# Optimization experiments

Hardware: AMD Instinct MI355X
Metric: run time of the kernel (lower is better)

## Reference

```python
import jax, jax.numpy as jnp
import numpy as np

D = 1024      # d_model
H = 2         # num_heads
DH = D // H   # head dim


def setup_inputs() -> dict:
    key = jax.random.key(0)
    ks = jax.random.split(key, 16)
    B, N = 512, 512
    s = 0.02
    return {
        "h": jax.random.normal(ks[0], (B, D), jnp.float32),
        "c": jax.random.normal(ks[1], (B, D), jnp.float32),
        "all_states": jax.random.normal(ks[2], (B, N, D), jnp.float32),
        "external_input": jax.random.normal(ks[3], (B, D), jnp.float32),
        # nn.MultiheadAttention params
        "in_proj_w": jax.random.normal(ks[4], (3 * D, D), jnp.float32) * s,
        "in_proj_b": jnp.zeros((3 * D,), jnp.float32),
        "out_proj_w": jax.random.normal(ks[5], (D, D), jnp.float32) * s,
        "out_proj_b": jnp.zeros((D,), jnp.float32),
        # nn.LSTMCell params (gate order: i, f, g, o)
        "w_ih": jax.random.normal(ks[6], (4 * D, 2 * D), jnp.float32) * s,
        "b_ih": jnp.zeros((4 * D,), jnp.float32),
        "w_hh": jax.random.normal(ks[7], (4 * D, D), jnp.float32) * s,
        "b_hh": jnp.zeros((4 * D,), jnp.float32),
        # ln_out params
        "ln_w": jnp.ones((D,), jnp.float32),
        "ln_b": jnp.zeros((D,), jnp.float32),
    }


def _layer_norm(x, w, b, eps=1e-5):
    mu = jnp.mean(x, axis=-1, keepdims=True)
    var = jnp.var(x, axis=-1, keepdims=True)
    return (x - mu) * jax.lax.rsqrt(var + eps) * w + b


def reference(h, c, all_states, external_input,
              in_proj_w, in_proj_b, out_proj_w, out_proj_b,
              w_ih, b_ih, w_hh, b_hh, ln_w, ln_b):
    B, N, _ = all_states.shape
    wq, wk, wv = in_proj_w[:D], in_proj_w[D:2 * D], in_proj_w[2 * D:]
    bq, bk, bv = in_proj_b[:D], in_proj_b[D:2 * D], in_proj_b[2 * D:]

    # single-query multi-head attention over all_states
    q = (h @ wq.T + bq).reshape(B, H, DH)                     # [B,H,Dh]
    k = (all_states @ wk.T + bk).reshape(B, N, H, DH)          # [B,N,H,Dh]
    v = (all_states @ wv.T + bv).reshape(B, N, H, DH)
    scores = jnp.einsum("bhd,bnhd->bhn", q, k) / jnp.sqrt(jnp.float32(DH))
    attn = jax.nn.softmax(scores, axis=-1)                     # [B,H,N]
    ctx = jnp.einsum("bhn,bnhd->bhd", attn, v).reshape(B, D)
    context = ctx @ out_proj_w.T + out_proj_b                  # [B,D]

    # LSTMCell on cat([context, external_input])
    rnn_in = jnp.concatenate([context, external_input], axis=-1)  # [B,2D]
    gates = rnn_in @ w_ih.T + b_ih + h @ w_hh.T + b_hh            # [B,4D]
    i, f, g, o = jnp.split(gates, 4, axis=-1)
    new_c = jax.nn.sigmoid(f) * c + jax.nn.sigmoid(i) * jnp.tanh(g)
    new_h = jax.nn.sigmoid(o) * jnp.tanh(new_c)

    return _layer_norm(new_h, ln_w, ln_b), new_c
```

## Files before the change

### kernel.cpp

```cpp
#include <hip/hip_runtime.h>
#include <math.h>
#include <stdint.h>

constexpr int kD  = 1024;
constexpr int kB  = 512;
constexpr int kN  = 512;
constexpr int kDH = 512;

using bf16x8 = __attribute__((ext_vector_type(8))) short;
using f32x4v = __attribute__((ext_vector_type(4))) float;
using us8    = __attribute__((ext_vector_type(8))) unsigned short;
using us4    = __attribute__((ext_vector_type(4))) unsigned short;

__device__ __forceinline__ unsigned short f2bf(float f) {
    uint32_t u = __float_as_uint(f);
    u += 0x7fffu + ((u >> 16) & 1u);
    return (unsigned short)(u >> 16);
}

__device__ __forceinline__ float bf2f(unsigned short s) {
    return __uint_as_float((uint32_t)s << 16);
}

__device__ __forceinline__ void async16(const void* g, void* l) {
    __builtin_amdgcn_global_load_lds(
        (const __attribute__((address_space(1))) uint32_t*)g,
        (__attribute__((address_space(3))) uint32_t*)l, 16, 0, 0);
}

__global__ __launch_bounds__(256)
void cvt_bf16(const float* __restrict__ src, unsigned short* __restrict__ dst,
              int scols8, int dcols, int coloff, int n8)
{
    int idx = blockIdx.x * 256 + threadIdx.x;
    if (idx >= n8) return;
    int row = idx / scols8;
    int c = (idx - row * scols8) * 8;
    const float4* s = (const float4*)(src + (long)row * ((long)scols8 * 8) + c);
    float4 v0 = s[0], v1 = s[1];
    us8 o;
    o[0] = f2bf(v0.x); o[1] = f2bf(v0.y); o[2] = f2bf(v0.z); o[3] = f2bf(v0.w);
    o[4] = f2bf(v1.x); o[5] = f2bf(v1.y); o[6] = f2bf(v1.z); o[7] = f2bf(v1.w);
    *(us8*)(dst + (long)row * dcols + coloff + c) = o;
}

__global__ __launch_bounds__(256)
void tcvt_wk(const float* __restrict__ wk, unsigned short* __restrict__ dst)
{
    __shared__ float t[32][33];
    const int nt = blockIdx.x;
    const int kt = blockIdx.y;
    const int hh = blockIdx.z;
    const int tx = threadIdx.x & 31, ty = threadIdx.x >> 5;
    const float scale = 0.044194173824159216f;
#pragma unroll
    for (int j = 0; j < 4; ++j)
        t[ty + j * 8][tx] = wk[(long)(hh * 512 + kt * 32 + ty + j * 8) * kD + nt * 32 + tx];
    __syncthreads();
#pragma unroll
    for (int j = 0; j < 4; ++j) {
        int n = nt * 32 + ty + j * 8;
        int k = kt * 32 + tx;
        dst[(long)hh * 524288 + (long)n * 512 + k] = f2bf(t[tx][ty + j * 8] * scale);
    }
}

__global__ __launch_bounds__(256)
void badd_kernel(const float* __restrict__ a, const float* __restrict__ b,
                 float* __restrict__ o)
{
    int i = blockIdx.x * 256 + threadIdx.x;
    if (i < 4096) o[i] = a[i] + b[i];
}

__global__ __launch_bounds__(256)
void gemm_bf16(const unsigned short* __restrict__ A, int lda, long sAz,
               const unsigned short* __restrict__ B, int ldb, long sBz,
               float* __restrict__ Cf, int ldcf, long sCfz,
               unsigned short* __restrict__ Cb, int ldcb, long sCbz,
               const float* __restrict__ bias, long sbz, int K)
{
    __shared__ short As[4][64][8];
    __shared__ short Bs[4][128][8];
    A += (long)blockIdx.z * sAz;
    B += (long)blockIdx.z * sBz;

    const int tid = threadIdx.x;
    const int l = tid & 63, w = tid >> 6;
    const int wr = w >> 1, wc = w & 1;
    const int bm = blockIdx.y * 64, bn = blockIdx.x * 128;

    f32x4v acc[2][4] = {};

    for (int k0 = 0; k0 < K; k0 += 32) {
        __syncthreads();
        {
            int ks = tid >> 6, r = tid & 63;
            async16(A + (long)(bm + r) * lda + k0 + ks * 8, (short*)As + (long)tid * 8);
        }
#pragma unroll
        for (int j = 0; j < 2; ++j) {
            int ca = j * 256 + tid;
            int ks = ca >> 7, r = ca & 127;
            async16(B + (long)(bn + r) * ldb + k0 + ks * 8, (short*)Bs + (long)ca * 8);
        }
        __syncthreads();

        const int ks = l >> 4, rr = l & 15;
        bf16x8 a[2], b[4];
#pragma unroll
        for (int t = 0; t < 2; ++t)
            a[t] = *(const bf16x8*)&As[ks][wr * 32 + t * 16 + rr][0];
#pragma unroll
        for (int t = 0; t < 4; ++t)
            b[t] = *(const bf16x8*)&Bs[ks][wc * 64 + t * 16 + rr][0];
#pragma unroll
        for (int mt = 0; mt < 2; ++mt)
#pragma unroll
            for (int nt = 0; nt < 4; ++nt)
                acc[mt][nt] = __builtin_amdgcn_mfma_f32_16x16x32_bf16(
                    a[mt], b[nt], acc[mt][nt], 0, 0, 0);
    }

    const int rr = l & 15, rg = l >> 4;
#pragma unroll
    for (int mt = 0; mt < 2; ++mt) {
#pragma unroll
        for (int nt = 0; nt < 4; ++nt) {
            const int n = bn + wc * 64 + nt * 16 + rr;
            float bb = bias ? bias[(long)blockIdx.z * sbz + n] : 0.f;
#pragma unroll
            for (int r = 0; r < 4; ++r) {
                const int m = bm + wr * 32 + mt * 16 + rg * 4 + r;
                float val = acc[mt][nt][r] + bb;
                if (Cf) Cf[(long)blockIdx.z * sCfz + (long)m * ldcf + n] = val;
                if (Cb) Cb[(long)blockIdx.z * sCbz + (long)m * ldcb + n] = f2bf(val);
            }
        }
    }
}

__global__ __launch_bounds__(512, 4)
void attn7(const float* __restrict__ xall,
           const float* __restrict__ qt,
           unsigned short* __restrict__ spart_bf,
           float* __restrict__ mlpart)
{
    const int b = blockIdx.x;
    const int tid = threadIdx.x;
    const int w = tid >> 6, l = tid & 63;

    float qa[16], qb[16];
    {
        const float* qp = qt + (long)b * 2048 + l * 4;
#pragma unroll
        for (int q = 0; q < 4; ++q) {
            float4 v0 = *(const float4*)(qp + q * 256);
            float4 v1 = *(const float4*)(qp + 1024 + q * 256);
            qa[q*4+0] = v0.x; qa[q*4+1] = v0.y; qa[q*4+2] = v0.z; qa[q*4+3] = v0.w;
            qb[q*4+0] = v1.x; qb[q*4+1] = v1.y; qb[q*4+2] = v1.z; qb[q*4+3] = v1.w;
        }
    }

    float m0 = -1e30f, l0 = 0.f, m1 = -1e30f, l1 = 0.f;
    float sa[16] = {}, sb[16] = {};

    const float* xr = xall + ((long)b * kN + w * 64) * kD + l * 4;

    for (int r = 0; r < 64; ++r) {
        float xv[16];
#pragma unroll
        for (int q = 0; q < 4; ++q) {
            float4 v = *(const float4*)(xr + q * 256);
            xv[q*4+0] = v.x; xv[q*4+1] = v.y; xv[q*4+2] = v.z; xv[q*4+3] = v.w;
        }
        xr += kD;

        float c0=0.f,c1=0.f,c2=0.f,c3=0.f, e0=0.f,e1=0.f,e2=0.f,e3=0.f;
#pragma unroll
        for (int q = 0; q < 4; ++q) {
            c0 += xv[q*4+0]*qa[q*4+0]; c1 += xv[q*4+1]*qa[q*4+1];
            c2 += xv[q*4+2]*qa[q*4+2]; c3 += xv[q*4+3]*qa[q*4+3];
            e0 += xv[q*4+0]*qb[q*4+0]; e1 += xv[q*4+1]*qb[q*4+1];
            e2 += xv[q*4+2]*qb[q*4+2]; e3 += xv[q*4+3]*qb[q*4+3];
        }
        float d0 = (c0 + c1) + (c2 + c3);
        float d1 = (e0 + e1) + (e2 + e3);
#pragma unroll
        for (int mm = 32; mm >= 1; mm >>= 1) {
            d0 += __shfl_xor(d0, mm);
            d1 += __shfl_xor(d1, mm);
        }

        if (d0 > m0 + 8.f) {
            float rsc = __expf(m0 - d0);
            l0 *= rsc;
#pragma unroll
            for (int j = 0; j < 16; ++j) sa[j] *= rsc;
            m0 = d0;
        }
        float p0 = __expf(d0 - m0);
        l0 += p0;

        if (d1 > m1 + 8.f) {
            float rsc = __expf(m1 - d1);
            l1 *= rsc;
#pragma unroll
            for (int j = 0; j < 16; ++j) sb[j] *= rsc;
            m1 = d1;
        }
        float p1 = __expf(d1 - m1);
        l1 += p1;

#pragma unroll
        for (int j = 0; j < 16; ++j) {
            sa[j] += p0 * xv[j];
            sb[j] += p1 * xv[j];
        }
    }

    unsigned short* sp0 = spart_bf + (((long)b * 8 + w) * 2 + 0) * 1024 + l * 4;
    unsigned short* sp1 = spart_bf + (((long)b * 8 + w) * 2 + 1) * 1024 + l * 4;
#pragma unroll
    for (int q = 0; q < 4; ++q) {
        us4 o0, o1;
        o0[0] = f2bf(sa[q*4+0]); o0[1] = f2bf(sa[q*4+1]);
        o0[2] = f2bf(sa[q*4+2]); o0[3] = f2bf(sa[q*4+3]);
        o1[0] = f2bf(sb[q*4+0]); o1[1] = f2bf(sb[q*4+1]);
        o1[2] = f2bf(sb[q*4+2]); o1[3] = f2bf(sb[q*4+3]);
        *(us4*)(sp0 + q * 256) = o0;
        *(us4*)(sp1 + q * 256) = o1;
    }

    if (l == 0) {
        float* mlp = mlpart + (((long)b * 8 + w) * 2) * 2;
        mlp[0] = m0; mlp[1] = l0; mlp[2] = m1; mlp[3] = l1;
    }
}

__global__ __launch_bounds__(256)
void attn_combine8(const unsigned short* __restrict__ spart_bf,
                   const float* __restrict__ mlpart,
                   unsigned short* __restrict__ sac_bf)
{
    const int b = blockIdx.x;
    const int tid = threadIdx.x;
    const int h = tid >> 7, d0 = (tid & 127) * 8;

    float m[8], lv[8];
#pragma unroll
    for (int c = 0; c < 8; ++c) {
        const float* mlp = mlpart + (((long)b * 8 + c) * 2 + h) * 2;
        m[c] = mlp[0]; lv[c] = mlp[1];
    }
    float ms = m[0];
#pragma unroll
    for (int c = 1; c < 8; ++c) ms = fmaxf(ms, m[c]);
    float wgt[8], L = 0.f;
#pragma unroll
    for (int c = 0; c < 8; ++c) { wgt[c] = __expf(m[c] - ms); L += wgt[c] * lv[c]; }
    const float inv = 1.0f / L;

    float acc[8] = {};
#pragma unroll
    for (int c = 0; c < 8; ++c) {
        us8 sv = *(const us8*)(spart_bf + (((long)b * 8 + c) * 2 + h) * 1024 + d0);
#pragma unroll
        for (int j = 0; j < 8; ++j)
            acc[j] += wgt[c] * bf2f(sv[j]);
    }
    us8 o;
#pragma unroll
    for (int j = 0; j < 8; ++j) o[j] = f2bf(acc[j] * inv);
    *(us8*)(sac_bf + (long)b * 2048 + h * kD + d0) = o;
}

__device__ __forceinline__ float sigm(float x) { return 1.0f / (1.0f + __expf(-x)); }

__global__ __launch_bounds__(256)
void lstm_ln(const float* __restrict__ gates, const float* __restrict__ cin,
             const float* __restrict__ ln_w, const float* __restrict__ ln_b,
             float* __restrict__ out0, float* __restrict__ out1)
{
    __shared__ float red[2][4];
    __shared__ float stats[2];

    const int b = blockIdx.x;
    const int tid = threadIdx.x;
    const int d4 = tid * 4;
    const float* g = gates + (long)b * 4096;

    float4 gi = *(const float4*)(g + d4);
    float4 gf = *(const float4*)(g + 1024 + d4);
    float4 gg = *(const float4*)(g + 2048 + d4);
    float4 go = *(const float4*)(g + 3072 + d4);
    float4 cv = *(const float4*)(cin + (long)b * kD + d4);

    float iv[4] = {gi.x, gi.y, gi.z, gi.w};
    float fv[4] = {gf.x, gf.y, gf.z, gf.w};
    float gv[4] = {gg.x, gg.y, gg.z, gg.w};
    float ov[4] = {go.x, go.y, go.z, go.w};
    float cc[4] = {cv.x, cv.y, cv.z, cv.w};

    float nc[4], nh[4];
#pragma unroll
    for (int u = 0; u < 4; ++u) {
        nc[u] = sigm(fv[u]) * cc[u] + sigm(iv[u]) * tanhf(gv[u]);
        nh[u] = sigm(ov[u]) * tanhf(nc[u]);
    }
    *(float4*)(out1 + (long)b * kD + d4) = make_float4(nc[0], nc[1], nc[2], nc[3]);

    float sum = nh[0] + nh[1] + nh[2] + nh[3];
    float ss  = nh[0]*nh[0] + nh[1]*nh[1] + nh[2]*nh[2] + nh[3]*nh[3];
#pragma unroll
    for (int m = 32; m >= 1; m >>= 1) {
        sum += __shfl_xor(sum, m);
        ss  += __shfl_xor(ss, m);
    }
    const int wave = tid >> 6, lane = tid & 63;
    if (lane == 0) { red[0][wave] = sum; red[1][wave] = ss; }
    __syncthreads();
    if (tid == 0) {
        float s = red[0][0] + red[0][1] + red[0][2] + red[0][3];
        float q = red[1][0] + red[1][1] + red[1][2] + red[1][3];
        float mu = s / (float)kD;
        float var = q / (float)kD - mu * mu;
        stats[0] = mu;
        stats[1] = rsqrtf(var + 1e-5f);
    }
    __syncthreads();
    const float mu = stats[0], rstd = stats[1];
    float4 lw = *(const float4*)(ln_w + d4);
    float4 lb = *(const float4*)(ln_b + d4);
    float lwv[4] = {lw.x, lw.y, lw.z, lw.w};
    float lbv[4] = {lb.x, lb.y, lb.z, lb.w};
    float o[4];
#pragma unroll
    for (int u = 0; u < 4; ++u)
        o[u] = (nh[u] - mu) * rstd * lwv[u] + lbv[u];
    *(float4*)(out0 + (long)b * kD + d4) = make_float4(o[0], o[1], o[2], o[3]);
}

extern "C" void kernel_launch(void* const* d_in, const int* in_sizes, int n_in,
                              void* d_out, int out_size, void* d_ws, size_t ws_size,
                              hipStream_t stream)
{
    (void)in_sizes; (void)n_in; (void)out_size;

    const float* h    = (const float*)d_in[0];
    const float* c    = (const float*)d_in[1];
    const float* xall = (const float*)d_in[2];
    const float* ext  = (const float*)d_in[3];
    const float* in_w = (const float*)d_in[4];
    const float* in_b = (const float*)d_in[5];
    const float* wo   = (const float*)d_in[6];
    const float* bo   = (const float*)d_in[7];
    const float* w_ih = (const float*)d_in[8];
    const float* b_ih = (const float*)d_in[9];
    const float* w_hh = (const float*)d_in[10];
    const float* b_hh = (const float*)d_in[11];
    const float* ln_w = (const float*)d_in[12];
    const float* ln_b = (const float*)d_in[13];

    float* out0 = (float*)d_out;
    float* out1 = out0 + (long)kB * kD;

    char* p = (char*)d_ws;
    const size_t need = 63062016ull;
    if (ws_size < need) return;

    float*          badd   = (float*)p;          p += 16384;
    unsigned short* h_bf   = (unsigned short*)p; p += 1048576;
    unsigned short* wq_bf  = (unsigned short*)p; p += 2097152;
    unsigned short* wkT_bf = (unsigned short*)p; p += 2097152;
    unsigned short* wv_bf  = (unsigned short*)p; p += 2097152;
    unsigned short* wo_bf  = (unsigned short*)p; p += 2097152;
    unsigned short* q_bf   = (unsigned short*)p; p += 1048576;
    unsigned short* sac_bf = (unsigned short*)p; p += 2097152;
    unsigned short* ctx_bf = (unsigned short*)p; p += 1048576;
    unsigned short* acat   = (unsigned short*)p; p += 3145728;
    unsigned short* wcat   = (unsigned short*)p; p += 25165824;
    char* ov = p;
    float*          qtl      = (float*)ov;
    unsigned short* spart_bf = (unsigned short*)(ov + 4194304);
    float*          mlpart   = (float*)(ov + 4194304 + 16777216);
    float*          gates    = (float*)ov;

    const float* wk_f = in_w + (long)kD * kD;
    const float* bq = in_b;
    const float* bv = in_b + 2 * kD;

    auto cvt = [&](const float* src, unsigned short* dst, int rows, int scols,
                   int dcols, int coloff) {
        int n8 = rows * (scols / 8);
        cvt_bf16<<<(n8 + 255) / 256, 256, 0, stream>>>(src, dst, scols / 8, dcols, coloff, n8);
    };

    badd_kernel<<<16, 256, 0, stream>>>(b_ih, b_hh, badd);
    cvt(h, h_bf, 512, 1024, 1024, 0);
    cvt(in_w, wq_bf, 1024, 1024, 1024, 0);
    tcvt_wk<<<dim3(32, 16, 2), 256, 0, stream>>>(wk_f, wkT_bf);
    cvt(in_w + 2L * kD * kD, wv_bf, 1024, 1024, 1024, 0);
    cvt(wo, wo_bf, 1024, 1024, 1024, 0);
    cvt(w_ih, wcat, 4096, 2048, 3072, 0);
    cvt(w_hh, wcat, 4096, 1024, 3072, 2048);

    gemm_bf16<<<dim3(8, 8, 1), 256, 0, stream>>>(
        h_bf, 1024, 0, wq_bf, 1024, 0,
        nullptr, 0, 0, q_bf, 1024, 0, bq, 0, 1024);

    gemm_bf16<<<dim3(8, 8, 2), 256, 0, stream>>>(
        q_bf, 1024, 512, wkT_bf, 512, 524288,
        qtl, 2048, 1024, nullptr, 0, 0, nullptr, 0, 512);

    attn7<<<kB, 512, 0, stream>>>(xall, qtl, spart_bf, mlpart);

    attn_combine8<<<kB, 256, 0, stream>>>(spart_bf, mlpart, sac_bf);

    gemm_bf16<<<dim3(4, 8, 2), 256, 0, stream>>>(
        sac_bf, 2048, 1024, wv_bf, 1024, 524288,
        nullptr, 0, 0, ctx_bf, 1024, 512, bv, 512, 1024);

    gemm_bf16<<<dim3(8, 8, 1), 256, 0, stream>>>(
        ctx_bf, 1024, 0, wo_bf, 1024, 0,
        nullptr, 0, 0, acat, 3072, 0, bo, 0, 1024);

    cvt(ext, acat, 512, 1024, 3072, 1024);
    cvt(h,   acat, 512, 1024, 3072, 2048);

    gemm_bf16<<<dim3(32, 8, 1), 256, 0, stream>>>(
        acat, 3072, 0, wcat, 3072, 0,
        gates, 4096, 0, nullptr, 0, 0, badd, 0, 3072);

    lstm_ln<<<kB, 256, 0, stream>>>(gates, c, ln_w, ln_b, out0, out1);
}
```

Measured before the change: 445.0 us.

## Shrink small GEMM tiles to 64x64, deepen gates GEMM K-step, fuse bias add

The small 1024-wide GEMMs now use a 64x64 tile instead of 64x128, doubling the block count so more of the GPU's compute units are occupied. The large gates GEMM gets its own kernel that stages a K-slice of 64 per iteration, halving the number of barrier pairs, and adds b_ih+b_hh directly in the epilogue. That removes the separate bias-add kernel launch. The trade-offs are less operand reuse per block in the small GEMMs and more shared memory per block in the gates kernel.

```diff
diff --git a/kernel.cpp b/kernel.cpp
--- a/kernel.cpp
+++ b/kernel.cpp
@@ -66,58 +66,44 @@
 }
 
 __global__ __launch_bounds__(256)
-void badd_kernel(const float* __restrict__ a, const float* __restrict__ b,
-                 float* __restrict__ o)
-{
-    int i = blockIdx.x * 256 + threadIdx.x;
-    if (i < 4096) o[i] = a[i] + b[i];
-}
-
-__global__ __launch_bounds__(256)
-void gemm_bf16(const unsigned short* __restrict__ A, int lda, long sAz,
-               const unsigned short* __restrict__ B, int ldb, long sBz,
-               float* __restrict__ Cf, int ldcf, long sCfz,
-               unsigned short* __restrict__ Cb, int ldcb, long sCbz,
-               const float* __restrict__ bias, long sbz, int K)
+void gemm64(const unsigned short* __restrict__ A, int lda, long sAz,
+            const unsigned short* __restrict__ B, int ldb, long sBz,
+            float* __restrict__ Cf, int ldcf, long sCfz,
+            unsigned short* __restrict__ Cb, int ldcb, long sCbz,
+            const float* __restrict__ bias, long sbz, int K)
 {
     __shared__ short As[4][64][8];
-    __shared__ short Bs[4][128][8];
+    __shared__ short Bs[4][64][8];
     A += (long)blockIdx.z * sAz;
     B += (long)blockIdx.z * sBz;
 
     const int tid = threadIdx.x;
     const int l = tid & 63, w = tid >> 6;
     const int wr = w >> 1, wc = w & 1;
-    const int bm = blockIdx.y * 64, bn = blockIdx.x * 128;
-
-    f32x4v acc[2][4] = {};
+    const int bm = blockIdx.y * 64, bn = blockIdx.x * 64;
+
+    f32x4v acc[2][2] = {};
 
     for (int k0 = 0; k0 < K; k0 += 32) {
         __syncthreads();
         {
             int ks = tid >> 6, r = tid & 63;
             async16(A + (long)(bm + r) * lda + k0 + ks * 8, (short*)As + (long)tid * 8);
-        }
-#pragma unroll
-        for (int j = 0; j < 2; ++j) {
-            int ca = j * 256 + tid;
-            int ks = ca >> 7, r = ca & 127;
-            async16(B + (long)(bn + r) * ldb + k0 + ks * 8, (short*)Bs + (long)ca * 8);
+            async16(B + (long)(bn + r) * ldb + k0 + ks * 8, (short*)Bs + (long)tid * 8);
         }
         __syncthreads();
 
         const int ks = l >> 4, rr = l & 15;
-        bf16x8 a[2], b[4];
-#pragma unroll
-        for (int t = 0; t < 2; ++t)
+        bf16x8 a[2], b[2];
+#pragma unroll
+        for (int t = 0; t < 2; ++t) {
             a[t] = *(const bf16x8*)&As[ks][wr * 32 + t * 16 + rr][0];
-#pragma unroll
-        for (int t = 0; t < 4; ++t)
-            b[t] = *(const bf16x8*)&Bs[ks][wc * 64 + t * 16 + rr][0];
+            b[t] = *(const bf16x8*)&Bs[ks][wc * 32 + t * 16 + rr][0];
+        }
 #pragma unroll
         for (int mt = 0; mt < 2; ++mt)
 #pragma unroll
-            for (int nt = 0; nt < 4; ++nt)
+            for (int nt = 0; nt < 2; ++nt)
                 acc[mt][nt] = __builtin_amdgcn_mfma_f32_16x16x32_bf16(
                     a[mt], b[nt], acc[mt][nt], 0, 0, 0);
     }
@@ -126,8 +112,8 @@
 #pragma unroll
     for (int mt = 0; mt < 2; ++mt) {
 #pragma unroll
-        for (int nt = 0; nt < 4; ++nt) {
-            const int n = bn + wc * 64 + nt * 16 + rr;
+        for (int nt = 0; nt < 2; ++nt) {
+            const int n = bn + wc * 32 + nt * 16 + rr;
             float bb = bias ? bias[(long)blockIdx.z * sbz + n] : 0.f;
 #pragma unroll
             for (int r = 0; r < 4; ++r) {
@@ -135,6 +121,74 @@
                 float val = acc[mt][nt][r] + bb;
                 if (Cf) Cf[(long)blockIdx.z * sCfz + (long)m * ldcf + n] = val;
                 if (Cb) Cb[(long)blockIdx.z * sCbz + (long)m * ldcb + n] = f2bf(val);
+            }
+        }
+    }
+}
+
+__global__ __launch_bounds__(256)
+void gemm_gates(const unsigned short* __restrict__ A, int lda,
+                const unsigned short* __restrict__ B, int ldb,
+                float* __restrict__ Cf, int ldcf,
+                const float* __restrict__ b1, const float* __restrict__ b2,
+                int K)
+{
+    __shared__ short As[8][64][8];
+    __shared__ short Bs[8][128][8];
+
+    const int tid = threadIdx.x;
+    const int l = tid & 63, w = tid >> 6;
+    const int wr = w >> 1, wc = w & 1;
+    const int bm = blockIdx.y * 64, bn = blockIdx.x * 128;
+
+    f32x4v acc[2][4] = {};
+
+    for (int k0 = 0; k0 < K; k0 += 64) {
+        __syncthreads();
+#pragma unroll
+        for (int j = 0; j < 2; ++j) {
+            int ca = j * 256 + tid;
+            int ks = ca >> 6, r = ca & 63;
+            async16(A + (long)(bm + r) * lda + k0 + ks * 8, (short*)As + (long)ca * 8);
+        }
+#pragma unroll
+        for (int j = 0; j < 4; ++j) {
+            int ca = j * 256 + tid;
+            int ks = ca >> 7, r = ca & 127;
+            async16(B + (long)(bn + r) * ldb + k0 + ks * 8, (short*)Bs + (long)ca * 8);
+        }
+        __syncthreads();
+
+        const int ksl = l >> 4, rr = l & 15;
+#pragma unroll
+        for (int p = 0; p < 2; ++p) {
+            bf16x8 a[2], b[4];
+#pragma unroll
+            for (int t = 0; t < 2; ++t)
+                a[t] = *(const bf16x8*)&As[p * 4 + ksl][wr * 32 + t * 16 + rr][0];
+#pragma unroll
+            for (int t = 0; t < 4; ++t)
+                b[t] = *(const bf16x8*)&Bs[p * 4 + ksl][wc * 64 + t * 16 + rr][0];
+#pragma unroll
+            for (int mt = 0; mt < 2; ++mt)
+#pragma unroll
+                for (int nt = 0; nt < 4; ++nt)
+                    acc[mt][nt] = __builtin_amdgcn_mfma_f32_16x16x32_bf16(
+                        a[mt], b[nt], acc[mt][nt], 0, 0, 0);
+        }
+    }
+
+    const int rr = l & 15, rg = l >> 4;
+#pragma unroll
+    for (int mt = 0; mt < 2; ++mt) {
+#pragma unroll
+        for (int nt = 0; nt < 4; ++nt) {
+            const int n = bn + wc * 64 + nt * 16 + rr;
+            const float bb = b1[n] + b2[n];
+#pragma unroll
+            for (int r = 0; r < 4; ++r) {
+                const int m = bm + wr * 32 + mt * 16 + rg * 4 + r;
+                Cf[(long)m * ldcf + n] = acc[mt][nt][r] + bb;
             }
         }
     }
@@ -369,7 +423,7 @@
     const size_t need = 63062016ull;
     if (ws_size < need) return;
 
-    float*          badd   = (float*)p;          p += 16384;
+    p += 16384;
     unsigned short* h_bf   = (unsigned short*)p; p += 1048576;
     unsigned short* wq_bf  = (unsigned short*)p; p += 2097152;
     unsigned short* wkT_bf = (unsigned short*)p; p += 2097152;
@@ -396,7 +450,6 @@
         cvt_bf16<<<(n8 + 255) / 256, 256, 0, stream>>>(src, dst, scols / 8, dcols, coloff, n8);
     };
 
-    badd_kernel<<<16, 256, 0, stream>>>(b_ih, b_hh, badd);
     cvt(h, h_bf, 512, 1024, 1024, 0);
     cvt(in_w, wq_bf, 1024, 1024, 1024, 0);
     tcvt_wk<<<dim3(32, 16, 2), 256, 0, stream>>>(wk_f, wkT_bf);
@@ -405,11 +458,11 @@
     cvt(w_ih, wcat, 4096, 2048, 3072, 0);
     cvt(w_hh, wcat, 4096, 1024, 3072, 2048);
 
-    gemm_bf16<<<dim3(8, 8, 1), 256, 0, stream>>>(
+    gemm64<<<dim3(16, 8, 1), 256, 0, stream>>>(
         h_bf, 1024, 0, wq_bf, 1024, 0,
         nullptr, 0, 0, q_bf, 1024, 0, bq, 0, 1024);
 
-    gemm_bf16<<<dim3(8, 8, 2), 256, 0, stream>>>(
+    gemm64<<<dim3(16, 8, 2), 256, 0, stream>>>(
         q_bf, 1024, 512, wkT_bf, 512, 524288,
         qtl, 2048, 1024, nullptr, 0, 0, nullptr, 0, 512);
 
@@ -417,20 +470,19 @@
 
     attn_combine8<<<kB, 256, 0, stream>>>(spart_bf, mlpart, sac_bf);
 
-    gemm_bf16<<<dim3(4, 8, 2), 256, 0, stream>>>(
+    gemm64<<<dim3(8, 8, 2), 256, 0, stream>>>(
         sac_bf, 2048, 1024, wv_bf, 1024, 524288,
         nullptr, 0, 0, ctx_bf, 1024, 512, bv, 512, 1024);
 
-    gemm_bf16<<<dim3(8, 8, 1), 256, 0, stream>>>(
+    gemm64<<<dim3(16, 8, 1), 256, 0, stream>>>(
         ctx_bf, 1024, 0, wo_bf, 1024, 0,
         nullptr, 0, 0, acat, 3072, 0, bo, 0, 1024);
 
     cvt(ext, acat, 512, 1024, 3072, 1024);
     cvt(h,   acat, 512, 1024, 3072, 2048);
 
-    gemm_bf16<<<dim3(32, 8, 1), 256, 0, stream>>>(
-        acat, 3072, 0, wcat, 3072, 0,
-        gates, 4096, 0, nullptr, 0, 0, badd, 0, 3072);
+    gemm_gates<<<dim3(32, 8), 256, 0, stream>>>(
+        acat, 3072, wcat, 3072, gates, 4096, b_ih, b_hh, 3072);
 
     lstm_ln<<<kB, 256, 0, stream>>>(gates, c, ln_w, ln_b, out0, out1);
 }
```

New measurement: 409.0 us. 8.1% less time.
